# Optimization experiments

Hardware: AMD Instinct MI355X
Metric: run time of the kernel (lower is better)

Reference implementation:

```python
import jax, jax.numpy as jnp
import numpy as np

N = 100_000      # nodes
E = 3_200_000    # edges (avg degree 32)
IN = 128         # in_dim
H = 64           # hidden
C = 2            # n_classes
G = 128          # graphs in batch


def setup_inputs() -> dict:
    key = jax.random.key(0)
    ks = jax.random.split(key, 14)
    x = jax.random.normal(ks[0], (N, IN), jnp.float32)
    edge_index = jax.random.randint(ks[1], (2, E), 0, N)
    edge_weight = jax.random.uniform(ks[2], (E,), jnp.float32)
    # deterministic sorted batch assignment -> every graph non-empty
    batch = (jnp.arange(N) * G) // N
    def lin(k, fi, fo):
        s = 1.0 / np.sqrt(fi)
        return jax.random.uniform(k, (fi, fo), jnp.float32, -s, s)
    return {
        "x": x, "edge_index": edge_index, "edge_weight": edge_weight,
        "batch": batch, "n_graphs": G,
        "W1": lin(ks[3], IN, H), "b1": jnp.zeros((H,), jnp.float32),
        "W2": lin(ks[4], H, H),  "b2": jnp.zeros((H,), jnp.float32),
        "pw": lin(ks[5], H, 1),  "pb": jnp.zeros((1,), jnp.float32),
        "lw1": lin(ks[6], 2 * H, H), "lb1": jnp.zeros((H,), jnp.float32),
        "lw2": lin(ks[7], H, C),     "lb2": jnp.zeros((C,), jnp.float32),
    }


def _gcn(x, edge_index, edge_weight, W, b):
    # PyG GCNConv with add_self_loops=False:
    # out = D^{-1/2} A D^{-1/2} (x W) + b, messages flow row->col
    h = x @ W                                   # [N, H]
    row, col = edge_index[0], edge_index[1]
    n = x.shape[0]
    deg = jax.ops.segment_sum(edge_weight, col, num_segments=n)
    dis = jnp.where(deg > 0, jax.lax.rsqrt(jnp.maximum(deg, 1e-12)), 0.0)
    norm = dis[row] * edge_weight * dis[col]    # [E]
    msg = h[row] * norm[:, None]                # [E, H] gather + scale
    out = jax.ops.segment_sum(msg, col, num_segments=n)  # scatter-add
    return out + b


def reference(x, edge_index, edge_weight, batch, n_graphs,
              W1, b1, W2, b2, pw, pb, lw1, lb1, lw2, lb2):
    h = jax.nn.relu(_gcn(x, edge_index, edge_weight, W1, b1))
    h = jax.nn.relu(_gcn(h, edge_index, edge_weight, W2, b2))
    # TopoPool (stand-in): learned per-node score gating (see notes)
    score = jax.nn.sigmoid(h @ pw + pb)         # [N, 1]
    h = h * score
    # global max pool || global mean pool per graph
    gmx = jax.ops.segment_max(h, batch, num_segments=n_graphs)
    gsum = jax.ops.segment_sum(h, batch, num_segments=n_graphs)
    cnt = jax.ops.segment_sum(jnp.ones((h.shape[0], 1), h.dtype), batch,
                              num_segments=n_graphs)
    gmean = gsum / jnp.maximum(cnt, 1.0)
    g = jnp.concatenate([gmx, gmean], axis=1)   # [G, 2H]
    g = jax.nn.relu(g @ lw1 + lb1)
    return g @ lw2 + lb2                        # [G, C]
```

## Files before the change

kernel.cpp:

```cpp
#include <hip/hip_runtime.h>
#include <math.h>


#define TPN_BLK 256
#define P1_EPT  32
#define P1_CHUNK (TPN_BLK * P1_EPT)
#define NB_MAX  512
#define BCAP    12288

__global__ __launch_bounds__(256)
void tpn_bin(const int* __restrict__ ei, const float* __restrict__ ew,
             int* __restrict__ binCur, uint2* __restrict__ binned,
             int E, int NB) {
    __shared__ uint2          sbuf[P1_CHUNK];
    __shared__ unsigned char  sbin2[P1_CHUNK];
    __shared__ unsigned char  sbinhi[P1_CHUNK / 8];
    __shared__ int hist[NB_MAX];
    __shared__ int loff[NB_MAX];
    __shared__ int lrank[NB_MAX];
    __shared__ int gbase[NB_MAX];
    __shared__ int ssc[256];

    int tid = threadIdx.x;
    for (int b = tid; b < NB_MAX; b += 256) { hist[b] = 0; lrank[b] = 0; }
    __syncthreads();

    int base = blockIdx.x * P1_CHUNK;
    uint2 ed[P1_EPT];
    short bn[P1_EPT];
    #pragma unroll
    for (int j = 0; j < P1_EPT; ++j) {
        int e = base + tid + j * 256;
        bn[j] = -1;
        if (e < E) {
            int r = ei[e], c = ei[E + e];
            bn[j] = (short)(c >> 8);
            ed[j] = make_uint2((unsigned)r | ((unsigned)(c & 255) << 17),
                               __float_as_uint(ew[e]));
            atomicAdd(&hist[bn[j]], 1);
        }
    }
    __syncthreads();
    {
        int b0 = 2 * tid, b1 = 2 * tid + 1;
        int h0 = hist[b0], h1 = hist[b1];
        int s = h0 + h1;
        ssc[tid] = s;
        __syncthreads();
        for (int st = 1; st < 256; st <<= 1) {
            int v = (tid >= st) ? ssc[tid - st] : 0;
            __syncthreads();
            ssc[tid] += v;
            __syncthreads();
        }
        int pre = ssc[tid] - s;
        loff[b0] = pre;
        loff[b1] = pre + h0;
    }
    __syncthreads();
    for (int b = tid; b < NB; b += 256) {
        int h = hist[b];
        if (h > 0) gbase[b] = atomicAdd(&binCur[b], h);
    }
    if (tid < P1_CHUNK / 8 / 256 * 256 || true) {
        for (int i = tid; i < P1_CHUNK / 8; i += 256) sbinhi[i] = 0;
    }
    __syncthreads();
    #pragma unroll
    for (int j = 0; j < P1_EPT; ++j) {
        if (bn[j] >= 0) {
            int p = loff[bn[j]] + atomicAdd(&lrank[bn[j]], 1);
            sbuf[p] = ed[j];
            sbin2[p] = (unsigned char)(bn[j] & 255);
            if (bn[j] >= 256) atomicOr((int*)&sbinhi[(p >> 3) & ~3],
                                       1 << ((p & 31)));
        }
    }
    __syncthreads();
    int m = min(E - base, P1_CHUNK);
    for (int i = tid; i < m; i += 256) {
        uint2 u = sbuf[i];
        int hi = (((const int*)sbinhi)[i >> 5] >> (i & 31)) & 1;
        int b = sbin2[i] + (hi << 8);
        int dst = gbase[b] + (i - loff[b]);
        if (dst < BCAP) binned[(size_t)b * BCAP + dst] = u;
    }
}

__global__ void tpn_binscan(const int* __restrict__ binCur, int* __restrict__ binOff,
                            int NB) {
    __shared__ int sh[NB_MAX];
    int t = threadIdx.x;
    int v = (t < NB) ? min(binCur[t], BCAP) : 0;
    sh[t] = v;
    __syncthreads();
    for (int st = 1; st < NB_MAX; st <<= 1) {
        int u = (t >= st) ? sh[t - st] : 0;
        __syncthreads();
        sh[t] += u;
        __syncthreads();
    }
    if (t < NB) binOff[t] = sh[t] - v;
}

__global__ void tpn_build(const uint2* __restrict__ binned, const int* __restrict__ binCur,
                          const int* __restrict__ binOff, uint2* __restrict__ packed,
                          int* __restrict__ off, int* __restrict__ cnt,
                          float* __restrict__ dis, int N) {
    __shared__ int   lcnt[256];
    __shared__ int   loff[256];
    __shared__ int   lrank[256];
    __shared__ int   lincl[256];
    __shared__ float ldeg[256];
    int b = blockIdx.x, tid = threadIdx.x;
    int m = min(binCur[b], BCAP);
    const uint2* src = binned + (size_t)b * BCAP;
    lcnt[tid] = 0; lrank[tid] = 0; ldeg[tid] = 0.0f;
    __syncthreads();
    for (int i = tid; i < m; i += 256) {
        uint2 u = src[i];
        int ln = u.x >> 17;
        atomicAdd(&lcnt[ln], 1);
        atomicAdd(&ldeg[ln], __uint_as_float(u.y));
    }
    __syncthreads();
    lincl[tid] = lcnt[tid];
    __syncthreads();
    for (int st = 1; st < 256; st <<= 1) {
        int u = (tid >= st) ? lincl[tid - st] : 0;
        __syncthreads();
        lincl[tid] += u;
        __syncthreads();
    }
    int excl = lincl[tid] - lcnt[tid];
    loff[tid] = excl;
    int node = (b << 8) + tid;
    if (node < N) {
        off[node] = binOff[b] + excl;
        cnt[node] = lcnt[tid];
        float s = ldeg[tid];
        dis[node] = (s > 0.0f) ? rsqrtf(fmaxf(s, 1e-12f)) : 0.0f;
    }
    __syncthreads();
    int gbase = binOff[b];
    for (int i = tid; i < m; i += 256) {
        uint2 u = src[i];
        int ln = u.x >> 17;
        int rk = atomicAdd(&lrank[ln], 1);
        packed[gbase + loff[ln] + rk] = make_uint2(u.x & 0x1FFFF, u.y);
    }
}

__global__ __launch_bounds__(256, 4)
void tpn_gemm_t(const float* __restrict__ X, const float* __restrict__ W,
                const float* __restrict__ dis, float* __restrict__ Y,
                int N, int K) {
    __shared__ float sX[64][68];
    __shared__ float sW[64][64];
    const int t  = threadIdx.x;
    const int r  = t >> 4;
    const int cc = t & 15;
    const int fg = t & 15;
    const int ng = t >> 4;
    const int nb = blockIdx.x * 64;

    float acc[4][4] = {{0.f}};

    for (int kc = 0; kc < K; kc += 64) {
        __syncthreads();
        #pragma unroll
        for (int p = 0; p < 4; ++p) {
            int n = nb + r + p * 16;
            int ns = (n < N) ? n : (N - 1);
            float4 v = *reinterpret_cast<const float4*>(X + (size_t)ns * K + kc + 4 * cc);
            *reinterpret_cast<float4*>(&sX[r + p * 16][4 * cc]) = v;
        }
        #pragma unroll
        for (int p = 0; p < 4; ++p) {
            int k = kc + r + p * 16;
            float4 v = *reinterpret_cast<const float4*>(W + (size_t)k * 64 + 4 * cc);
            *reinterpret_cast<float4*>(&sW[r + p * 16][4 * cc]) = v;
        }
        __syncthreads();
        #pragma unroll 4
        for (int k = 0; k < 64; ++k) {
            float4 wv = *reinterpret_cast<const float4*>(&sW[k][4 * fg]);
            float x0 = sX[4 * ng + 0][k];
            float x1 = sX[4 * ng + 1][k];
            float x2 = sX[4 * ng + 2][k];
            float x3 = sX[4 * ng + 3][k];
            acc[0][0] = fmaf(x0, wv.x, acc[0][0]);
            acc[0][1] = fmaf(x0, wv.y, acc[0][1]);
            acc[0][2] = fmaf(x0, wv.z, acc[0][2]);
            acc[0][3] = fmaf(x0, wv.w, acc[0][3]);
            acc[1][0] = fmaf(x1, wv.x, acc[1][0]);
            acc[1][1] = fmaf(x1, wv.y, acc[1][1]);
            acc[1][2] = fmaf(x1, wv.z, acc[1][2]);
            acc[1][3] = fmaf(x1, wv.w, acc[1][3]);
            acc[2][0] = fmaf(x2, wv.x, acc[2][0]);
            acc[2][1] = fmaf(x2, wv.y, acc[2][1]);
            acc[2][2] = fmaf(x2, wv.z, acc[2][2]);
            acc[2][3] = fmaf(x2, wv.w, acc[2][3]);
            acc[3][0] = fmaf(x3, wv.x, acc[3][0]);
            acc[3][1] = fmaf(x3, wv.y, acc[3][1]);
            acc[3][2] = fmaf(x3, wv.z, acc[3][2]);
            acc[3][3] = fmaf(x3, wv.w, acc[3][3]);
        }
    }
    #pragma unroll
    for (int i = 0; i < 4; ++i) {
        int n = nb + 4 * ng + i;
        if (n < N) {
            float d = dis[n];
            float4 v = make_float4(acc[i][0] * d, acc[i][1] * d,
                                   acc[i][2] * d, acc[i][3] * d);
            *reinterpret_cast<float4*>(Y + (size_t)n * 64 + 4 * fg) = v;
        }
    }
}

template <bool FUSE_SCORE>
__global__ __launch_bounds__(256)
void tpn_agg(const uint2* __restrict__ packed, const int* __restrict__ off,
             const int* __restrict__ cnt, const float* __restrict__ dis,
             const float* __restrict__ Hin, const float* __restrict__ bias,
             const float* __restrict__ pw, const float* __restrict__ pb,
             float* __restrict__ Hout, int N) {
    int wid = (blockIdx.x * blockDim.x + threadIdx.x) >> 6;
    int lane = threadIdx.x & 63;
    if (wid >= N) return;
    const int eg = lane >> 4;
    const int fb = (lane & 15) * 4;
    int start = off[wid], n = cnt[wid];
    const uint2* b = packed + start;
    const float* hp = Hin + fb;
    float dc = dis[wid];

    float4 A0 = {0.f, 0.f, 0.f, 0.f};
    float4 A1 = {0.f, 0.f, 0.f, 0.f};
    float4 A2 = {0.f, 0.f, 0.f, 0.f};
    float4 A3 = {0.f, 0.f, 0.f, 0.f};
    int j = 0;
    for (; j + 16 <= n; j += 16) {
        uint2 p0 = b[j + eg];
        uint2 p1 = b[j + 4 + eg];
        uint2 p2 = b[j + 8 + eg];
        uint2 p3 = b[j + 12 + eg];
        float4 v0 = *reinterpret_cast<const float4*>(hp + (size_t)p0.x * 64);
        float4 v1 = *reinterpret_cast<const float4*>(hp + (size_t)p1.x * 64);
        float4 v2 = *reinterpret_cast<const float4*>(hp + (size_t)p2.x * 64);
        float4 v3 = *reinterpret_cast<const float4*>(hp + (size_t)p3.x * 64);
        float w0 = __uint_as_float(p0.y);
        float w1 = __uint_as_float(p1.y);
        float w2 = __uint_as_float(p2.y);
        float w3 = __uint_as_float(p3.y);
        A0.x = fmaf(w0, v0.x, A0.x); A0.y = fmaf(w0, v0.y, A0.y);
        A0.z = fmaf(w0, v0.z, A0.z); A0.w = fmaf(w0, v0.w, A0.w);
        A1.x = fmaf(w1, v1.x, A1.x); A1.y = fmaf(w1, v1.y, A1.y);
        A1.z = fmaf(w1, v1.z, A1.z); A1.w = fmaf(w1, v1.w, A1.w);
        A2.x = fmaf(w2, v2.x, A2.x); A2.y = fmaf(w2, v2.y, A2.y);
        A2.z = fmaf(w2, v2.z, A2.z); A2.w = fmaf(w2, v2.w, A2.w);
        A3.x = fmaf(w3, v3.x, A3.x); A3.y = fmaf(w3, v3.y, A3.y);
        A3.z = fmaf(w3, v3.z, A3.z); A3.w = fmaf(w3, v3.w, A3.w);
    }
    for (; j + 8 <= n; j += 8) {
        uint2 p0 = b[j + eg];
        uint2 p1 = b[j + 4 + eg];
        float4 v0 = *reinterpret_cast<const float4*>(hp + (size_t)p0.x * 64);
        float4 v1 = *reinterpret_cast<const float4*>(hp + (size_t)p1.x * 64);
        float w0 = __uint_as_float(p0.y);
        float w1 = __uint_as_float(p1.y);
        A0.x = fmaf(w0, v0.x, A0.x); A0.y = fmaf(w0, v0.y, A0.y);
        A0.z = fmaf(w0, v0.z, A0.z); A0.w = fmaf(w0, v0.w, A0.w);
        A1.x = fmaf(w1, v1.x, A1.x); A1.y = fmaf(w1, v1.y, A1.y);
        A1.z = fmaf(w1, v1.z, A1.z); A1.w = fmaf(w1, v1.w, A1.w);
    }
    for (; j < n; j += 4) {
        int idx = j + eg;
        uint2 p = (idx < n) ? b[idx] : make_uint2(0u, 0u);
        float4 v = *reinterpret_cast<const float4*>(hp + (size_t)p.x * 64);
        float w = __uint_as_float(p.y);
        A0.x = fmaf(w, v.x, A0.x); A0.y = fmaf(w, v.y, A0.y);
        A0.z = fmaf(w, v.z, A0.z); A0.w = fmaf(w, v.w, A0.w);
    }
    float4 acc;
    acc.x = (A0.x + A1.x) + (A2.x + A3.x);
    acc.y = (A0.y + A1.y) + (A2.y + A3.y);
    acc.z = (A0.z + A1.z) + (A2.z + A3.z);
    acc.w = (A0.w + A1.w) + (A2.w + A3.w);
    acc.x += __shfl_xor(acc.x, 16); acc.x += __shfl_xor(acc.x, 32);
    acc.y += __shfl_xor(acc.y, 16); acc.y += __shfl_xor(acc.y, 32);
    acc.z += __shfl_xor(acc.z, 16); acc.z += __shfl_xor(acc.z, 32);
    acc.w += __shfl_xor(acc.w, 16); acc.w += __shfl_xor(acc.w, 32);

    const float4 bv = *reinterpret_cast<const float4*>(bias + fb);
    float4 h;
    h.x = fmaxf(fmaf(acc.x, dc, bv.x), 0.0f);
    h.y = fmaxf(fmaf(acc.y, dc, bv.y), 0.0f);
    h.z = fmaxf(fmaf(acc.z, dc, bv.z), 0.0f);
    h.w = fmaxf(fmaf(acc.w, dc, bv.w), 0.0f);
    if (FUSE_SCORE) {
        const float4 pv = *reinterpret_cast<const float4*>(pw + fb);
        float t = h.x * pv.x + h.y * pv.y + h.z * pv.z + h.w * pv.w;
        #pragma unroll
        for (int m = 1; m <= 8; m <<= 1) t += __shfl_xor(t, m);
        float s = 1.0f / (1.0f + expf(-(t + pb[0])));
        h.x *= s; h.y *= s; h.z *= s; h.w *= s;
    }
    if (eg == 0)
        *reinterpret_cast<float4*>(Hout + (size_t)wid * 64 + fb) = h;
}

__global__ void tpn_pool(const float* __restrict__ Hs, const int* __restrict__ batch,
                         int N, float* __restrict__ Gf) {
    int g = blockIdx.x;
    int s, e;
    {
        int lo = 0, hi = N;
        while (lo < hi) { int mid = (lo + hi) >> 1; if (batch[mid] < g) lo = mid + 1; else hi = mid; }
        s = lo;
        lo = 0; hi = N;
        while (lo < hi) { int mid = (lo + hi) >> 1; if (batch[mid] < g + 1) lo = mid + 1; else hi = mid; }
        e = lo;
    }
    int lane = threadIdx.x & 63;
    int w = threadIdx.x >> 6;
    float mx = -3.4e38f, sm = 0.0f;
    for (int i = s + w; i < e; i += 4) {
        float v = Hs[(size_t)i * 64 + lane];
        mx = fmaxf(mx, v);
        sm += v;
    }
    __shared__ float shm[4][64], shs[4][64];
    shm[w][lane] = mx; shs[w][lane] = sm;
    __syncthreads();
    if (w == 0) {
        mx = fmaxf(fmaxf(shm[0][lane], shm[1][lane]), fmaxf(shm[2][lane], shm[3][lane]));
        sm = shs[0][lane] + shs[1][lane] + shs[2][lane] + shs[3][lane];
        float c = (float)(e - s);
        float inv = 1.0f / fmaxf(c, 1.0f);
        Gf[g * 128 + lane]      = mx;
        Gf[g * 128 + 64 + lane] = sm * inv;
    }
}

__global__ void tpn_mlp(const float* __restrict__ Gf, const float* __restrict__ lw1,
                        const float* __restrict__ lb1, const float* __restrict__ lw2,
                        const float* __restrict__ lb2, float* __restrict__ out,
                        int G, int C) {
    int wid = (blockIdx.x * blockDim.x + threadIdx.x) >> 6;
    int lane = threadIdx.x & 63;
    if (wid >= G) return;
    const float* gr = Gf + (size_t)wid * 128;
    float acc = lb1[lane];
    for (int k = 0; k < 128; k += 4) {
        float4 gv = *reinterpret_cast<const float4*>(gr + k);
        acc = fmaf(gv.x, lw1[(k + 0) * 64 + lane], acc);
        acc = fmaf(gv.y, lw1[(k + 1) * 64 + lane], acc);
        acc = fmaf(gv.z, lw1[(k + 2) * 64 + lane], acc);
        acc = fmaf(gv.w, lw1[(k + 3) * 64 + lane], acc);
    }
    float t = fmaxf(acc, 0.0f);
    for (int c = 0; c < C; ++c) {
        float v = t * lw2[lane * C + c];
        #pragma unroll
        for (int m = 32; m > 0; m >>= 1) v += __shfl_xor(v, m);
        if (lane == 0) out[wid * C + c] = v + lb2[c];
    }
}

extern "C" void kernel_launch(void* const* d_in, const int* in_sizes, int n_in,
                              void* d_out, int out_size, void* d_ws, size_t ws_size,
                              hipStream_t stream) {
    const float* x   = (const float*)d_in[0];
    const int*   ei  = (const int*)  d_in[1];
    const float* ew  = (const float*)d_in[2];
    const int*   bat = (const int*)  d_in[3];
    const float* W1  = (const float*)d_in[5];
    const float* b1  = (const float*)d_in[6];
    const float* W2  = (const float*)d_in[7];
    const float* b2  = (const float*)d_in[8];
    const float* pw  = (const float*)d_in[9];
    const float* pb  = (const float*)d_in[10];
    const float* lw1 = (const float*)d_in[11];
    const float* lb1 = (const float*)d_in[12];
    const float* lw2 = (const float*)d_in[13];
    const float* lb2 = (const float*)d_in[14];
    float* out = (float*)d_out;

    const int N  = in_sizes[3];
    const int E  = in_sizes[2];
    const int IN = in_sizes[0] / N;
    const int C  = in_sizes[14];
    const int G  = out_size / C;
    const int NB = (N + 255) >> 8;

    char* ws = (char*)d_ws;
    size_t o = 0;
    auto alloc = [&](size_t bytes) { void* p = ws + o; o = (o + bytes + 255) & ~(size_t)255; return p; };
    int*   off    = (int*)  alloc((size_t)N * 4);
    int*   cnt    = (int*)  alloc((size_t)N * 4);
    float* dis    = (float*)alloc((size_t)N * 4);
    int*   binCur = (int*)  alloc((size_t)NB_MAX * 4);
    int*   binOff = (int*)  alloc((size_t)NB_MAX * 4);
    float* Gf     = (float*)alloc((size_t)G * 128 * 4);
    uint2* packed = (uint2*)alloc((size_t)E * 8);
    float* hA     = (float*)alloc((size_t)N * 64 * 4);
    float* hB     = (float*)alloc((size_t)N * 64 * 4);
    uint2* binned = (uint2*)hA;
    (void)n_in; (void)ws_size;

    (void)hipMemsetAsync(binCur, 0, (size_t)NB_MAX * 4, stream);

    const int p1b   = (E + P1_CHUNK - 1) / P1_CHUNK;
    const int ggrid = (N + 63) / 64;
    const int agrid = (N * 64 + TPN_BLK - 1) / TPN_BLK;

    tpn_bin<<<p1b, TPN_BLK, 0, stream>>>(ei, ew, binCur, binned, E, NB);
    tpn_binscan<<<1, NB_MAX, 0, stream>>>(binCur, binOff, NB);
    tpn_build<<<NB, 256, 0, stream>>>(binned, binCur, binOff, packed, off, cnt, dis, N);

    tpn_gemm_t<<<ggrid, 256, 0, stream>>>(x, W1, dis, hA, N, IN);
    tpn_agg<false><<<agrid, TPN_BLK, 0, stream>>>(packed, off, cnt, dis, hA, b1, pw, pb, hB, N);

    tpn_gemm_t<<<ggrid, 256, 0, stream>>>(hB, W2, dis, hA, N, 64);
    tpn_agg<true><<<agrid, TPN_BLK, 0, stream>>>(packed, off, cnt, dis, hA, b2, pw, pb, hB, N);

    tpn_pool<<<G, TPN_BLK, 0, stream>>>(hB, bat, N, Gf);
    tpn_mlp<<<(G * 64 + TPN_BLK - 1) / TPN_BLK, TPN_BLK, 0, stream>>>(Gf, lw1, lb1, lw2, lb2, out, G, C);
}
```

Baseline: 419.4 us.

## Fuse second-layer weight GEMM into first aggregation epilogue and simplify edge binning

The first aggregation kernel now multiplies each node's post-ReLU feature row by W2 and scales by the degree normalisation in its epilogue. It uses wave shuffles and per-lane W2 column loads, which removes the standalone second GEMM launch and its full read/write of the node feature buffer. The binning kernel halves edges per thread and stores a 16-bit bin id per slot instead of a byte plus a packed high-bit mask. That drops an atomicOr, a clear loop and a barrier, at the cost of more blocks and more global atomics on the bin counters. The fused epilogue adds 64 shuffles and 64 W2 loads per node inside the aggregation kernel.

```diff
diff --git a/kernel.cpp b/kernel.cpp
--- a/kernel.cpp
+++ b/kernel.cpp
@@ -3,7 +3,7 @@
 
 
 #define TPN_BLK 256
-#define P1_EPT  32
+#define P1_EPT  16
 #define P1_CHUNK (TPN_BLK * P1_EPT)
 #define NB_MAX  512
 #define BCAP    12288
@@ -13,8 +13,7 @@
              int* __restrict__ binCur, uint2* __restrict__ binned,
              int E, int NB) {
     __shared__ uint2          sbuf[P1_CHUNK];
-    __shared__ unsigned char  sbin2[P1_CHUNK];
-    __shared__ unsigned char  sbinhi[P1_CHUNK / 8];
+    __shared__ unsigned short sbin[P1_CHUNK];
     __shared__ int hist[NB_MAX];
     __shared__ int loff[NB_MAX];
     __shared__ int lrank[NB_MAX];
@@ -27,14 +26,14 @@
 
     int base = blockIdx.x * P1_CHUNK;
     uint2 ed[P1_EPT];
-    short bn[P1_EPT];
+    int   bn[P1_EPT];
     #pragma unroll
     for (int j = 0; j < P1_EPT; ++j) {
         int e = base + tid + j * 256;
         bn[j] = -1;
         if (e < E) {
             int r = ei[e], c = ei[E + e];
-            bn[j] = (short)(c >> 8);
+            bn[j] = c >> 8;
             ed[j] = make_uint2((unsigned)r | ((unsigned)(c & 255) << 17),
                                __float_as_uint(ew[e]));
             atomicAdd(&hist[bn[j]], 1);
@@ -62,26 +61,19 @@
         int h = hist[b];
         if (h > 0) gbase[b] = atomicAdd(&binCur[b], h);
     }
-    if (tid < P1_CHUNK / 8 / 256 * 256 || true) {
-        for (int i = tid; i < P1_CHUNK / 8; i += 256) sbinhi[i] = 0;
-    }
-    __syncthreads();
     #pragma unroll
     for (int j = 0; j < P1_EPT; ++j) {
         if (bn[j] >= 0) {
             int p = loff[bn[j]] + atomicAdd(&lrank[bn[j]], 1);
             sbuf[p] = ed[j];
-            sbin2[p] = (unsigned char)(bn[j] & 255);
-            if (bn[j] >= 256) atomicOr((int*)&sbinhi[(p >> 3) & ~3],
-                                       1 << ((p & 31)));
+            sbin[p] = (unsigned short)bn[j];
         }
     }
     __syncthreads();
     int m = min(E - base, P1_CHUNK);
     for (int i = tid; i < m; i += 256) {
         uint2 u = sbuf[i];
-        int hi = (((const int*)sbinhi)[i >> 5] >> (i & 31)) & 1;
-        int b = sbin2[i] + (hi << 8);
+        int b = sbin[i];
         int dst = gbase[b] + (i - loff[b]);
         if (dst < BCAP) binned[(size_t)b * BCAP + dst] = u;
     }
@@ -219,13 +211,13 @@
     }
 }
 
-template <bool FUSE_SCORE>
+template <bool FUSE_SCORE, bool FUSE_W2>
 __global__ __launch_bounds__(256)
 void tpn_agg(const uint2* __restrict__ packed, const int* __restrict__ off,
              const int* __restrict__ cnt, const float* __restrict__ dis,
              const float* __restrict__ Hin, const float* __restrict__ bias,
              const float* __restrict__ pw, const float* __restrict__ pb,
-             float* __restrict__ Hout, int N) {
+             const float* __restrict__ W2, float* __restrict__ Hout, int N) {
     int wid = (blockIdx.x * blockDim.x + threadIdx.x) >> 6;
     int lane = threadIdx.x & 63;
     if (wid >= N) return;
@@ -307,8 +299,24 @@
         float s = 1.0f / (1.0f + expf(-(t + pb[0])));
         h.x *= s; h.y *= s; h.z *= s; h.w *= s;
     }
-    if (eg == 0)
-        *reinterpret_cast<float4*>(Hout + (size_t)wid * 64 + fb) = h;
+    if (FUSE_W2) {
+        float a2 = 0.0f;
+        #pragma unroll
+        for (int q = 0; q < 16; ++q) {
+            float b0 = __shfl(h.x, q);
+            float b1 = __shfl(h.y, q);
+            float b2 = __shfl(h.z, q);
+            float b3 = __shfl(h.w, q);
+            a2 = fmaf(b0, W2[(4 * q + 0) * 64 + lane], a2);
+            a2 = fmaf(b1, W2[(4 * q + 1) * 64 + lane], a2);
+            a2 = fmaf(b2, W2[(4 * q + 2) * 64 + lane], a2);
+            a2 = fmaf(b3, W2[(4 * q + 3) * 64 + lane], a2);
+        }
+        Hout[(size_t)wid * 64 + lane] = dc * a2;
+    } else {
+        if (eg == 0)
+            *reinterpret_cast<float4*>(Hout + (size_t)wid * 64 + fb) = h;
+    }
 }
 
 __global__ void tpn_pool(const float* __restrict__ Hs, const int* __restrict__ batch,
@@ -421,11 +429,12 @@
     tpn_build<<<NB, 256, 0, stream>>>(binned, binCur, binOff, packed, off, cnt, dis, N);
 
     tpn_gemm_t<<<ggrid, 256, 0, stream>>>(x, W1, dis, hA, N, IN);
-    tpn_agg<false><<<agrid, TPN_BLK, 0, stream>>>(packed, off, cnt, dis, hA, b1, pw, pb, hB, N);
-
-    tpn_gemm_t<<<ggrid, 256, 0, stream>>>(hB, W2, dis, hA, N, 64);
-    tpn_agg<true><<<agrid, TPN_BLK, 0, stream>>>(packed, off, cnt, dis, hA, b2, pw, pb, hB, N);
-
-    tpn_pool<<<G, TPN_BLK, 0, stream>>>(hB, bat, N, Gf);
+    tpn_agg<false, true><<<agrid, TPN_BLK, 0, stream>>>(packed, off, cnt, dis, hA,
+                                                        b1, pw, pb, W2, hB, N);
+
+    tpn_agg<true, false><<<agrid, TPN_BLK, 0, stream>>>(packed, off, cnt, dis, hB,
+                                                        b2, pw, pb, W2, hA, N);
+
+    tpn_pool<<<G, TPN_BLK, 0, stream>>>(hA, bat, N, Gf);
     tpn_mlp<<<(G * 64 + TPN_BLK - 1) / TPN_BLK, TPN_BLK, 0, stream>>>(Gf, lw1, lb1, lw2, lb2, out, G, C);
 }
```

New measurement: 409.3 us. 1.02x faster.
